# Kernel tuning notes

Measured on AMD Instinct MI355X. Metric: run time of the kernel, lower is better.

The kernel has to match this reference:

```python
import jax, jax.numpy as jnp
import numpy as np

N_PTS = 2_097_152


def _pe(x):
    # num_frequencies = 3: [sin(pi x), cos(pi x), sin(2pi x), cos(2pi x), sin(4pi x), cos(4pi x)] -> [N,18]
    parts = []
    for i in range(3):
        f = np.float32((2.0 ** i) * np.pi)
        parts.append(jnp.sin(f * x))
        parts.append(jnp.cos(f * x))
    return jnp.concatenate(parts, axis=-1)


def _trilinear(vol, coords):
    # vol: [C,D,H,W]; coords: [N,3] in grid_sample order (x->W, y->H, z->D),
    # align_corners=False, zeros padding. Returns [C,N].
    C, D, H, W = vol.shape
    x = (coords[:, 0] + 1.0) * (W * 0.5) - 0.5
    y = (coords[:, 1] + 1.0) * (H * 0.5) - 0.5
    z = (coords[:, 2] + 1.0) * (D * 0.5) - 0.5
    x0f = jnp.floor(x); y0f = jnp.floor(y); z0f = jnp.floor(z)
    tx = x - x0f; ty = y - y0f; tz = z - z0f
    x0 = x0f.astype(jnp.int32); y0 = y0f.astype(jnp.int32); z0 = z0f.astype(jnp.int32)

    def corner(zi, yi, xi, w):
        valid = (zi >= 0) & (zi < D) & (yi >= 0) & (yi < H) & (xi >= 0) & (xi < W)
        v = vol[:, jnp.clip(zi, 0, D - 1), jnp.clip(yi, 0, H - 1), jnp.clip(xi, 0, W - 1)]
        return v * (w * valid)[None, :]

    return (corner(z0, y0, x0, (1 - tz) * (1 - ty) * (1 - tx))
            + corner(z0, y0, x0 + 1, (1 - tz) * (1 - ty) * tx)
            + corner(z0, y0 + 1, x0, (1 - tz) * ty * (1 - tx))
            + corner(z0, y0 + 1, x0 + 1, (1 - tz) * ty * tx)
            + corner(z0 + 1, y0, x0, tz * (1 - ty) * (1 - tx))
            + corner(z0 + 1, y0, x0 + 1, tz * (1 - ty) * tx)
            + corner(z0 + 1, y0 + 1, x0, tz * ty * (1 - tx))
            + corner(z0 + 1, y0 + 1, x0 + 1, tz * ty * tx))


def setup_inputs() -> dict:
    key = jax.random.key(0)
    ks = jax.random.split(key, 11)
    q = 1.0
    inp = {
        'x': jax.random.uniform(ks[0], (N_PTS, 3), dtype=jnp.float32),
        'grid0': jax.random.normal(ks[1], (4, 32, 32, 32), dtype=jnp.float32),
        'grid1': jax.random.normal(ks[2], (4, 64, 64, 64), dtype=jnp.float32),
        'grid2': jax.random.normal(ks[3], (2, 128, 128, 128), dtype=jnp.float32),
        'noise0': jax.random.uniform(ks[4], (4, 32, 32, 32), dtype=jnp.float32) / q - 0.5 / q,
        'noise1': jax.random.uniform(ks[5], (4, 64, 64, 64), dtype=jnp.float32) / q - 0.5 / q,
        'noise2': jax.random.uniform(ks[6], (2, 128, 128, 128), dtype=jnp.float32) / q - 0.5 / q,
        'w1': jax.random.normal(ks[7], (64, 20), dtype=jnp.float32) * (1.0 / np.sqrt(20.0)),
        'b1': jnp.zeros((64,), dtype=jnp.float32),
        'w2': jax.random.normal(ks[8], (7, 64), dtype=jnp.float32) * (1.0 / np.sqrt(64.0)),
        'b2': jnp.zeros((7,), dtype=jnp.float32),
    }
    return inp


def reference(x, grid0, grid1, grid2, noise0, noise1, noise2, w1, b1, w2, b2):
    pe = _pe(x)  # [N,18]
    feats = []
    for i, (g, nz) in enumerate(((grid0, noise0), (grid1, noise1), (grid2, noise2))):
        gv = g + nz  # training-mode noise injection, shared across the two samples
        feats.append(_trilinear(gv, pe[:, i * 6:i * 6 + 3]))
        feats.append(_trilinear(gv, pe[:, i * 6 + 3:i * 6 + 6]))
    f = jnp.concatenate(feats, axis=0).T  # [N,20]
    h = jax.nn.leaky_relu(f @ w1.T + b1, negative_slope=0.01)
    return h @ w2.T + b2  # [N,7]
```

## Files before the change

kernel.cpp:

```cpp
#include <hip/hip_runtime.h>


#define NB 16384
#define KB 128
#define NXCD 8

typedef _Float16 f16x2 __attribute__((ext_vector_type(2)));
typedef __fp16  h8    __attribute__((ext_vector_type(8)));
typedef float   f4    __attribute__((ext_vector_type(4)));

__device__ __forceinline__ f16x2 pkrtz(float a, float b) {
    return __builtin_bit_cast(f16x2, __builtin_amdgcn_cvt_pkrtz(a, b));
}
__device__ __forceinline__ unsigned pkrtzu(float a, float b) {
    return __builtin_bit_cast(unsigned, __builtin_amdgcn_cvt_pkrtz(a, b));
}
__device__ __forceinline__ float fdot2(f16x2 a, f16x2 b, float c) {
    return __builtin_amdgcn_fdot2(a, b, c, false);
}
__device__ __forceinline__ f16x2 u2h(unsigned u) { return __builtin_bit_cast(f16x2, u); }

__device__ __forceinline__ int bin_of(float xv, float yv, float zv) {
    int qx = min(max((int)(xv * 16.f), 0), 15);
    int qy = min(max((int)(yv * 32.f), 0), 31);
    int qz = min(max((int)(zv * 32.f), 0), 31);
    return (qz << 9) | (qy << 4) | qx;
}

#define PREP_BLOCKS 9568

__global__ __launch_bounds__(256)
void prep_k(const float* __restrict__ x,
            const float* __restrict__ g0, const float* __restrict__ n0,
            const float* __restrict__ g1, const float* __restrict__ n1,
            const float* __restrict__ g2, const float* __restrict__ n2,
            const float* __restrict__ w1, const float* __restrict__ w2,
            uint2* __restrict__ p0, uint2* __restrict__ p1,
            unsigned* __restrict__ p2,
            unsigned short* __restrict__ w1p, unsigned short* __restrict__ w2p,
            int* __restrict__ counts, int npts) {
    __shared__ unsigned h32[NB / 2];
    const int b = blockIdx.x, t = threadIdx.x;
    if (b < 8256) {
        int i = b * 256 + t;
        if (i < 2113536) {
            int z = i / 16512, rem = i % 16512;
            int y = rem / 129, xp = rem % 129;
            int v = (z * 128 + y) * 128 + max(xp - 1, 0);
            p2[i] = pkrtzu(g2[v] + n2[v], g2[2097152 + v] + n2[2097152 + v]);
        }
    } else if (b < 9296) {
        int i = (b - 8256) * 256 + t;
        if (i < 266240) {
            int z = i / 4160, rem = i % 4160;
            int y = rem / 65, xp = rem % 65;
            int v = (z * 64 + y) * 64 + max(xp - 1, 0);
            uint2 r;
            r.x = pkrtzu(g1[v] + n1[v], g1[262144 + v] + n1[262144 + v]);
            r.y = pkrtzu(g1[524288 + v] + n1[524288 + v], g1[786432 + v] + n1[786432 + v]);
            p1[i] = r;
        }
    } else if (b < 9428) {
        int i = (b - 9296) * 256 + t;
        if (i < 33792) {
            int z = i / 1056, rem = i % 1056;
            int y = rem / 33, xp = rem % 33;
            int v = (z * 32 + y) * 32 + max(xp - 1, 0);
            uint2 r;
            r.x = pkrtzu(g0[v] + n0[v], g0[32768 + v] + n0[32768 + v]);
            r.y = pkrtzu(g0[65536 + v] + n0[65536 + v], g0[98304 + v] + n0[98304 + v]);
            p0[i] = r;
        }
    } else if (b < 9556) {
        const int cb = b - 9428;
        for (int i = t; i < NB / 2; i += 256) h32[i] = 0u;
        __syncthreads();
        const int chunk = (npts + KB - 1) / KB;
        const int s = cb * chunk, e = min(s + chunk, npts);
        for (int p = s + t; p < e; p += 256) {
            int bin = bin_of(x[3 * p], x[3 * p + 1], x[3 * p + 2]);
            atomicAdd(&h32[bin >> 1], 1u << ((bin & 1) * 16));
        }
        __syncthreads();
        for (int i = t; i < NB; i += 256)
            counts[cb * NB + i] = (int)((h32[i >> 1] >> ((i & 1) * 16)) & 0xffffu);
    } else {
        int i = (b - 9556) * 256 + t;
        if (i < 2048) {
            int j = i >> 5, k = i & 31;
            float v = (k < 20) ? w1[j * 20 + k] : 0.f;
            w1p[i] = __builtin_bit_cast(unsigned short, (_Float16)v);
        } else if (i < 3072) {
            int i2 = i - 2048;
            int o = i2 >> 6, jj = i2 & 63;
            float v = (o < 7) ? w2[o * 64 + jj] : 0.f;
            w2p[i2] = __builtin_bit_cast(unsigned short, (_Float16)v);
        }
    }
}

__global__ __launch_bounds__(256)
void scan_rows_k(const int* __restrict__ counts, int* __restrict__ offs,
                 int* __restrict__ rowsum) {
    __shared__ int tile[KB][32];
    const int g = blockIdx.x, t = threadIdx.x;
    for (int idx = t; idx < KB * 32; idx += 256) {
        int b = idx >> 5, j = idx & 31;
        tile[b][j] = counts[b * NB + g * 32 + j];
    }
    __syncthreads();
    if (t < 32) {
        int run = 0;
#pragma unroll 8
        for (int b = 0; b < KB; ++b) {
            int v = tile[b][t];
            tile[b][t] = run;
            run += v;
        }
        rowsum[g * 32 + t] = run;
    }
    __syncthreads();
    for (int idx = t; idx < KB * 32; idx += 256) {
        int b = idx >> 5, j = idx & 31;
        offs[b * NB + g * 32 + j] = tile[b][j];
    }
}

__global__ __launch_bounds__(1024)
void scatter_k(const float* __restrict__ x, const int* __restrict__ offs,
               const int* __restrict__ rowsum, float4* __restrict__ sorted,
               int npts) {
    __shared__ int base[NB];
    __shared__ int sh[1024];
    const int t = threadIdx.x, b = blockIdx.x;

    int s16 = 0;
    for (int i = 0; i < 16; ++i) s16 += rowsum[t * 16 + i];
    sh[t] = s16;
    __syncthreads();
    for (int d = 1; d < 1024; d <<= 1) {
        int add = (t >= d) ? sh[t - d] : 0;
        __syncthreads();
        sh[t] += add;
        __syncthreads();
    }
    int run = sh[t] - s16;
    for (int i = 0; i < 16; ++i) {
        int v = rowsum[t * 16 + i];
        base[t * 16 + i] = run;
        run += v;
    }
    __syncthreads();
    for (int i = t; i < NB; i += 1024) base[i] += offs[b * NB + i];
    __syncthreads();

    const int chunk = (npts + KB - 1) / KB;
    const int s = b * chunk, e = min(s + chunk, npts);
    for (int p = s + t; p < e; p += 1024) {
        float xv = x[3 * p], yv = x[3 * p + 1], zv = x[3 * p + 2];
        int pos = atomicAdd(&base[bin_of(xv, yv, zv)], 1);
        float4 v; v.x = xv; v.y = yv; v.z = zv; v.w = __int_as_float(p);
        sorted[pos] = v;
    }
}

template<int S>
__device__ __forceinline__ void tl_setup(float cx, float cy, float cz,
        int& o00, int& o01, int& o10, int& o11,
        f16x2& w00, f16x2& w01, f16x2& w10, f16x2& w11) {
    const float hs = (float)S * 0.5f;
    float gx = fmaf(cx, hs, hs - 0.5f);
    float gy = fmaf(cy, hs, hs - 0.5f);
    float gz = fmaf(cz, hs, hs - 0.5f);
    float fx = floorf(gx), fy = floorf(gy), fz = floorf(gz);
    float tx = gx - fx, ty = gy - fy, tz = gz - fz;
    int x0 = (int)fx, y0 = (int)fy, z0 = (int)fz;
    float wx0 = (1.f - tx) * ((x0 >= 0)    ? 1.f : 0.f);
    float wx1 = tx         * ((x0 + 1 < S) ? 1.f : 0.f);
    float wy0 = (1.f - ty) * ((y0 >= 0)    ? 1.f : 0.f);
    float wy1 = ty         * ((y0 + 1 < S) ? 1.f : 0.f);
    float wz0 = (1.f - tz) * ((z0 >= 0)    ? 1.f : 0.f);
    float wz1 = tz         * ((z0 + 1 < S) ? 1.f : 0.f);
    const int xb = x0 + 1;
    f16x2 wx2 = pkrtz(wx0, wx1);
    int ys0 = max(y0, 0), ys1 = min(y0 + 1, S - 1);
    int zs0 = max(z0, 0), zs1 = min(z0 + 1, S - 1);
    o00 = (zs0 * S + ys0) * (S + 1) + xb;
    o01 = (zs0 * S + ys1) * (S + 1) + xb;
    o10 = (zs1 * S + ys0) * (S + 1) + xb;
    o11 = (zs1 * S + ys1) * (S + 1) + xb;
    float a00 = wz0 * wy0, a01 = wz0 * wy1, a10 = wz1 * wy0, a11 = wz1 * wy1;
    w00 = pkrtz(a00, a00) * wx2;
    w01 = pkrtz(a01, a01) * wx2;
    w10 = pkrtz(a10, a10) * wx2;
    w11 = pkrtz(a11, a11) * wx2;
}

struct TL4S {
    uint4 r00, r01, r10, r11;
    f16x2 w00, w01, w10, w11;
};
template<int S>
__device__ __forceinline__ TL4S tl4_issue(const uint2* __restrict__ vol,
                                          float cx, float cy, float cz) {
    TL4S r; int o00, o01, o10, o11;
    tl_setup<S>(cx, cy, cz, o00, o01, o10, o11, r.w00, r.w01, r.w10, r.w11);
    r.r00 = *reinterpret_cast<const uint4*>(vol + o00);
    r.r01 = *reinterpret_cast<const uint4*>(vol + o01);
    r.r10 = *reinterpret_cast<const uint4*>(vol + o10);
    r.r11 = *reinterpret_cast<const uint4*>(vol + o11);
    return r;
}
#define TL4_ROW(s, R, WP, f) { uint4 r = (s).R; \
    unsigned pc0 = __builtin_amdgcn_perm(r.z, r.x, 0x05040100u); \
    unsigned pc1 = __builtin_amdgcn_perm(r.z, r.x, 0x07060302u); \
    unsigned pc2 = __builtin_amdgcn_perm(r.w, r.y, 0x05040100u); \
    unsigned pc3 = __builtin_amdgcn_perm(r.w, r.y, 0x07060302u); \
    (f)[0] = fdot2((s).WP, u2h(pc0), (f)[0]); (f)[1] = fdot2((s).WP, u2h(pc1), (f)[1]); \
    (f)[2] = fdot2((s).WP, u2h(pc2), (f)[2]); (f)[3] = fdot2((s).WP, u2h(pc3), (f)[3]); }
__device__ __forceinline__ void tl4_consume(const TL4S& s, float* f) {
    TL4_ROW(s, r00, w00, f) TL4_ROW(s, r01, w01, f)
    TL4_ROW(s, r10, w10, f) TL4_ROW(s, r11, w11, f)
}

struct TL2S {
    uint2 r00, r01, r10, r11;
    f16x2 w00, w01, w10, w11;
};
template<int S>
__device__ __forceinline__ TL2S tl2_issue(const unsigned* __restrict__ vol,
                                          float cx, float cy, float cz) {
    TL2S r; int o00, o01, o10, o11;
    tl_setup<S>(cx, cy, cz, o00, o01, o10, o11, r.w00, r.w01, r.w10, r.w11);
    r.r00 = *reinterpret_cast<const uint2*>(vol + o00);
    r.r01 = *reinterpret_cast<const uint2*>(vol + o01);
    r.r10 = *reinterpret_cast<const uint2*>(vol + o10);
    r.r11 = *reinterpret_cast<const uint2*>(vol + o11);
    return r;
}
#define TL2_ROW(s, R, WP, f) { uint2 r = (s).R; \
    unsigned pc0 = __builtin_amdgcn_perm(r.y, r.x, 0x05040100u); \
    unsigned pc1 = __builtin_amdgcn_perm(r.y, r.x, 0x07060302u); \
    (f)[0] = fdot2((s).WP, u2h(pc0), (f)[0]); (f)[1] = fdot2((s).WP, u2h(pc1), (f)[1]); }
__device__ __forceinline__ void tl2_consume(const TL2S& s, float* f) {
    TL2_ROW(s, r00, w00, f) TL2_ROW(s, r01, w01, f)
    TL2_ROW(s, r10, w10, f) TL2_ROW(s, r11, w11, f)
}

__device__ __forceinline__ void trig3(float x, float y, float z,
        float* s1, float* c1, float* s2, float* c2, float* s4, float* c4) {
    const float v[3] = {x, y, z};
#pragma unroll
    for (int d = 0; d < 3; ++d) {
        float sa = __builtin_amdgcn_sinf(0.5f * v[d]);
        float ca = __builtin_amdgcn_cosf(0.5f * v[d]);
        s1[d] = sa; c1[d] = ca;
        float sb = 2.f * sa * ca, cb = fmaf(-2.f * sa, sa, 1.f);
        s2[d] = sb; c2[d] = cb;
        s4[d] = 2.f * sb * cb; c4[d] = fmaf(-2.f * sb, sb, 1.f);
    }
}

__global__ __launch_bounds__(256, 3)
void motion_grid_main(const float4* __restrict__ sorted,
                      const float* __restrict__ xraw,
                      const uint2* __restrict__ g0v,
                      const uint2* __restrict__ g1v,
                      const unsigned* __restrict__ g2v,
                      const unsigned short* __restrict__ w1p_,
                      const unsigned short* __restrict__ w2p_,
                      const float* __restrict__ b1,
                      const float* __restrict__ b2,
                      float* __restrict__ out, int npts, int sortedMode,
                      int nblk) {
    __shared__ __align__(16) char smem[4 * 7424];
    int bid = blockIdx.x;
    if ((nblk & (NXCD - 1)) == 0) {
        int cpx = nblk / NXCD;
        bid = (bid % NXCD) * cpx + bid / NXCD;
    }
    const int tid = threadIdx.x;
    const int w = tid >> 6, l = tid & 63, c = l & 15, g = l >> 4;
    char* wbase = smem + w * 7424;
    const int p = bid * 256 + tid;

    float xv = 0.f, yv = 0.f, zv = 0.f;
    int orig = -1;
    if (p < npts) {
        if (sortedMode) {
            float4 sp = sorted[p];
            xv = sp.x; yv = sp.y; zv = sp.z; orig = __float_as_int(sp.w);
        } else {
            xv = xraw[3 * p]; yv = xraw[3 * p + 1]; zv = xraw[3 * p + 2];
            orig = p;
        }
    }
    float s1[3], c1[3], s2[3], c2[3], s4[3], c4[3];
    trig3(xv, yv, zv, s1, c1, s2, c2, s4, c4);

    TL4S S0s = tl4_issue<32>(g0v, s1[0], s1[1], s1[2]);
    TL4S S0c = tl4_issue<32>(g0v, c1[0], c1[1], c1[2]);
    TL4S S1s = tl4_issue<64>(g1v, s2[0], s2[1], s2[2]);
    TL4S S1c = tl4_issue<64>(g1v, c2[0], c2[1], c2[2]);
    TL2S S2s = tl2_issue<128>(g2v, s4[0], s4[1], s4[2]);
    TL2S S2c = tl2_issue<128>(g2v, c4[0], c4[1], c4[2]);

    float f[20];
#pragma unroll
    for (int i = 0; i < 20; ++i) f[i] = 0.f;
    tl4_consume(S0s, f + 0);  tl4_consume(S0c, f + 4);
    tl4_consume(S1s, f + 8);  tl4_consume(S1c, f + 12);
    tl2_consume(S2s, f + 16); tl2_consume(S2c, f + 18);
    {
        uint4* fs = (uint4*)(wbase + l * 80);
        fs[0] = make_uint4(pkrtzu(f[0], f[1]), pkrtzu(f[2], f[3]),
                           pkrtzu(f[4], f[5]), pkrtzu(f[6], f[7]));
        fs[1] = make_uint4(pkrtzu(f[8], f[9]), pkrtzu(f[10], f[11]),
                           pkrtzu(f[12], f[13]), pkrtzu(f[14], f[15]));
        fs[2] = make_uint4(pkrtzu(f[16], f[17]), pkrtzu(f[18], f[19]), 0u, 0u);
        fs[3] = make_uint4(0u, 0u, 0u, 0u);
    }

    h8 a1f0 = *(const h8*)(w1p_ + (0 * 16 + c) * 32 + g * 8);
    h8 a1f1 = *(const h8*)(w1p_ + (1 * 16 + c) * 32 + g * 8);
    h8 a1f2 = *(const h8*)(w1p_ + (2 * 16 + c) * 32 + g * 8);
    h8 a1f3 = *(const h8*)(w1p_ + (3 * 16 + c) * 32 + g * 8);
    f4 b1f0 = *(const f4*)(b1 + 0 * 16 + g * 4);
    f4 b1f1 = *(const f4*)(b1 + 1 * 16 + g * 4);
    f4 b1f2 = *(const f4*)(b1 + 2 * 16 + g * 4);
    f4 b1f3 = *(const f4*)(b1 + 3 * 16 + g * 4);
    h8 a20 = *(const h8*)(w2p_ + c * 64 + g * 8);
    h8 a21 = *(const h8*)(w2p_ + c * 64 + 32 + g * 8);
    float b2f0 = (g * 4 + 0 < 7) ? b2[g * 4 + 0] : 0.f;
    float b2f1 = (g * 4 + 1 < 7) ? b2[g * 4 + 1] : 0.f;
    float b2f2 = (g * 4 + 2 < 7) ? b2[g * 4 + 2] : 0.f;
    float b2f3 = (g * 4 + 3 < 7) ? b2[g * 4 + 3] : 0.f;

    const f4 zero4 = {0.f, 0.f, 0.f, 0.f};
#pragma unroll
    for (int n = 0; n < 4; ++n) {
        h8 bn = *(const h8*)(wbase + (n * 16 + c) * 80 + g * 16);
        __builtin_amdgcn_s_setprio(1);
        f4 d0 = __builtin_amdgcn_mfma_f32_16x16x32_f16(a1f0, bn, zero4, 0, 0, 0);
        f4 d1 = __builtin_amdgcn_mfma_f32_16x16x32_f16(a1f1, bn, zero4, 0, 0, 0);
        f4 d2m = __builtin_amdgcn_mfma_f32_16x16x32_f16(a1f2, bn, zero4, 0, 0, 0);
        f4 d3 = __builtin_amdgcn_mfma_f32_16x16x32_f16(a1f3, bn, zero4, 0, 0, 0);
        __builtin_amdgcn_s_setprio(0);
        d0 += b1f0; d1 += b1f1; d2m += b1f2; d3 += b1f3;
        {
            float h0 = fmaxf(d0[0], 0.01f * d0[0]), h1 = fmaxf(d0[1], 0.01f * d0[1]);
            float h2 = fmaxf(d0[2], 0.01f * d0[2]), h3 = fmaxf(d0[3], 0.01f * d0[3]);
            *(uint2*)(wbase + 5120 + c * 144 + 0 * 32 + g * 8) =
                make_uint2(pkrtzu(h0, h1), pkrtzu(h2, h3));
            h0 = fmaxf(d1[0], 0.01f * d1[0]); h1 = fmaxf(d1[1], 0.01f * d1[1]);
            h2 = fmaxf(d1[2], 0.01f * d1[2]); h3 = fmaxf(d1[3], 0.01f * d1[3]);
            *(uint2*)(wbase + 5120 + c * 144 + 1 * 32 + g * 8) =
                make_uint2(pkrtzu(h0, h1), pkrtzu(h2, h3));
            h0 = fmaxf(d2m[0], 0.01f * d2m[0]); h1 = fmaxf(d2m[1], 0.01f * d2m[1]);
            h2 = fmaxf(d2m[2], 0.01f * d2m[2]); h3 = fmaxf(d2m[3], 0.01f * d2m[3]);
            *(uint2*)(wbase + 5120 + c * 144 + 2 * 32 + g * 8) =
                make_uint2(pkrtzu(h0, h1), pkrtzu(h2, h3));
            h0 = fmaxf(d3[0], 0.01f * d3[0]); h1 = fmaxf(d3[1], 0.01f * d3[1]);
            h2 = fmaxf(d3[2], 0.01f * d3[2]); h3 = fmaxf(d3[3], 0.01f * d3[3]);
            *(uint2*)(wbase + 5120 + c * 144 + 3 * 32 + g * 8) =
                make_uint2(pkrtzu(h0, h1), pkrtzu(h2, h3));
        }
        h8 hb0 = *(const h8*)(wbase + 5120 + c * 144 + g * 16);
        h8 hb1 = *(const h8*)(wbase + 5120 + c * 144 + 64 + g * 16);
        __builtin_amdgcn_s_setprio(1);
        f4 o2 = __builtin_amdgcn_mfma_f32_16x16x32_f16(a20, hb0, zero4, 0, 0, 0);
        o2 = __builtin_amdgcn_mfma_f32_16x16x32_f16(a21, hb1, o2, 0, 0, 0);
        __builtin_amdgcn_s_setprio(0);
        int og = __shfl(orig, n * 16 + c, 64);
        if (og >= 0 && g < 2) {
            float* op = out + (size_t)og * 7 + g * 4;
            op[0] = o2[0] + b2f0;
            op[1] = o2[1] + b2f1;
            op[2] = o2[2] + b2f2;
            if (g == 0) op[3] = o2[3] + b2f3;
        }
    }
}

extern "C" void kernel_launch(void* const* d_in, const int* in_sizes, int n_in,
                              void* d_out, int out_size, void* d_ws, size_t ws_size,
                              hipStream_t stream) {
    const float* x  = (const float*)d_in[0];
    const float* g0 = (const float*)d_in[1];
    const float* g1 = (const float*)d_in[2];
    const float* g2 = (const float*)d_in[3];
    const float* n0 = (const float*)d_in[4];
    const float* n1 = (const float*)d_in[5];
    const float* n2 = (const float*)d_in[6];
    const float* w1 = (const float*)d_in[7];
    const float* b1 = (const float*)d_in[8];
    const float* w2 = (const float*)d_in[9];
    const float* b2 = (const float*)d_in[10];
    float* out = (float*)d_out;

    const int npts = in_sizes[0] / 3;

    char* ws = (char*)d_ws;
    size_t cur = 0;
    auto alloc = [&](size_t bytes) {
        char* p = ws + cur;
        cur = (cur + bytes + 255) & ~(size_t)255;
        return p;
    };
    uint2*          p0       = (uint2*)         alloc(33792u   * 8 + 64);
    uint2*          p1       = (uint2*)         alloc(266240u  * 8 + 64);
    unsigned*       p2       = (unsigned*)      alloc(2113536u * 4 + 64);
    unsigned short* w1p      = (unsigned short*)alloc(2048 * 2);
    unsigned short* w2p      = (unsigned short*)alloc(1024 * 2);
    int*            counts   = (int*)           alloc((size_t)KB * NB * 4);
    int*            offs     = (int*)           alloc((size_t)KB * NB * 4);
    int*            rowsum   = (int*)           alloc(NB * 4);
    float4*         sorted   = (float4*)        alloc((size_t)npts * 16);
    const int useSorted = (ws_size >= cur) ? 1 : 0;

    prep_k<<<PREP_BLOCKS, 256, 0, stream>>>(x, g0, n0, g1, n1, g2, n2, w1, w2,
                                            p0, p1, p2, w1p, w2p, counts, npts);
    if (useSorted) {
        scan_rows_k<<<NB / 32, 256, 0, stream>>>(counts, offs, rowsum);
        scatter_k<<<KB, 1024, 0, stream>>>(x, offs, rowsum, sorted, npts);
    }

    const int nblk = (npts + 255) / 256;
    motion_grid_main<<<nblk, 256, 0, stream>>>(
        sorted, x, p0, p1, p2, w1p, w2p, b1, b2, out, npts, useSorted, nblk);
}
```

Baseline: 198.8 us.

## Refine spatial binning to 32K bins and split histogram into its own kernel

Changes the point-sorting grid from 16x32x32 to 8x64x64 bins (32768 total) for finer y/z locality in the later trilinear gathers. Moves the histogram out of prep_k into a separate 1024-thread kernel, reuses the counts buffer in place for offsets instead of a separate offs array, and replaces the block-wide scan in scatter_k with a wavefront shuffle scan. This adds a kernel launch and doubles the per-block count traffic and the LDS use of scatter_k, in exchange for potentially better cache locality in the main kernel.

Result: faster. 172.1 us, median of 2 (-13.4%).

```diff
diff --git a/kernel.cpp b/kernel.cpp
--- a/kernel.cpp
+++ b/kernel.cpp
@@ -1,7 +1,7 @@
 #include <hip/hip_runtime.h>
 
 
-#define NB 16384
+#define NB 32768
 #define KB 128
 #define NXCD 8
 
@@ -21,25 +21,22 @@
 __device__ __forceinline__ f16x2 u2h(unsigned u) { return __builtin_bit_cast(f16x2, u); }
 
 __device__ __forceinline__ int bin_of(float xv, float yv, float zv) {
-    int qx = min(max((int)(xv * 16.f), 0), 15);
-    int qy = min(max((int)(yv * 32.f), 0), 31);
-    int qz = min(max((int)(zv * 32.f), 0), 31);
-    return (qz << 9) | (qy << 4) | qx;
-}
-
-#define PREP_BLOCKS 9568
+    int qx = min(max((int)(xv * 8.f), 0), 7);
+    int qy = min(max((int)(yv * 64.f), 0), 63);
+    int qz = min(max((int)(zv * 64.f), 0), 63);
+    return (qz << 9) | (qy << 3) | qx;
+}
+
+#define PREP_BLOCKS 9440
 
 __global__ __launch_bounds__(256)
-void prep_k(const float* __restrict__ x,
-            const float* __restrict__ g0, const float* __restrict__ n0,
+void prep_k(const float* __restrict__ g0, const float* __restrict__ n0,
             const float* __restrict__ g1, const float* __restrict__ n1,
             const float* __restrict__ g2, const float* __restrict__ n2,
             const float* __restrict__ w1, const float* __restrict__ w2,
             uint2* __restrict__ p0, uint2* __restrict__ p1,
             unsigned* __restrict__ p2,
-            unsigned short* __restrict__ w1p, unsigned short* __restrict__ w2p,
-            int* __restrict__ counts, int npts) {
-    __shared__ unsigned h32[NB / 2];
+            unsigned short* __restrict__ w1p, unsigned short* __restrict__ w2p) {
     const int b = blockIdx.x, t = threadIdx.x;
     if (b < 8256) {
         int i = b * 256 + t;
@@ -71,21 +68,8 @@
             r.y = pkrtzu(g0[65536 + v] + n0[65536 + v], g0[98304 + v] + n0[98304 + v]);
             p0[i] = r;
         }
-    } else if (b < 9556) {
-        const int cb = b - 9428;
-        for (int i = t; i < NB / 2; i += 256) h32[i] = 0u;
-        __syncthreads();
-        const int chunk = (npts + KB - 1) / KB;
-        const int s = cb * chunk, e = min(s + chunk, npts);
-        for (int p = s + t; p < e; p += 256) {
-            int bin = bin_of(x[3 * p], x[3 * p + 1], x[3 * p + 2]);
-            atomicAdd(&h32[bin >> 1], 1u << ((bin & 1) * 16));
-        }
-        __syncthreads();
-        for (int i = t; i < NB; i += 256)
-            counts[cb * NB + i] = (int)((h32[i >> 1] >> ((i & 1) * 16)) & 0xffffu);
     } else {
-        int i = (b - 9556) * 256 + t;
+        int i = (b - 9428) * 256 + t;
         if (i < 2048) {
             int j = i >> 5, k = i & 31;
             float v = (k < 20) ? w1[j * 20 + k] : 0.f;
@@ -99,9 +83,25 @@
     }
 }
 
+__global__ __launch_bounds__(1024)
+void hist_k(const float* __restrict__ x, int* __restrict__ counts, int npts) {
+    __shared__ unsigned h32[NB / 2];
+    const int t = threadIdx.x, b = blockIdx.x;
+    for (int i = t; i < NB / 2; i += 1024) h32[i] = 0u;
+    __syncthreads();
+    const int chunk = (npts + KB - 1) / KB;
+    const int s = b * chunk, e = min(s + chunk, npts);
+    for (int p = s + t; p < e; p += 1024) {
+        int bin = bin_of(x[3 * p], x[3 * p + 1], x[3 * p + 2]);
+        atomicAdd(&h32[bin >> 1], 1u << ((bin & 1) * 16));
+    }
+    __syncthreads();
+    for (int i = t; i < NB; i += 1024)
+        counts[b * NB + i] = (int)((h32[i >> 1] >> ((i & 1) * 16)) & 0xffffu);
+}
+
 __global__ __launch_bounds__(256)
-void scan_rows_k(const int* __restrict__ counts, int* __restrict__ offs,
-                 int* __restrict__ rowsum) {
+void scan_rows_k(int* __restrict__ counts, int* __restrict__ rowsum) {
     __shared__ int tile[KB][32];
     const int g = blockIdx.x, t = threadIdx.x;
     for (int idx = t; idx < KB * 32; idx += 256) {
@@ -122,7 +122,7 @@
     __syncthreads();
     for (int idx = t; idx < KB * 32; idx += 256) {
         int b = idx >> 5, j = idx & 31;
-        offs[b * NB + g * 32 + j] = tile[b][j];
+        counts[b * NB + g * 32 + j] = tile[b][j];
     }
 }
 
@@ -131,23 +131,29 @@
                const int* __restrict__ rowsum, float4* __restrict__ sorted,
                int npts) {
     __shared__ int base[NB];
-    __shared__ int sh[1024];
+    __shared__ int wsum[16];
     const int t = threadIdx.x, b = blockIdx.x;
-
-    int s16 = 0;
-    for (int i = 0; i < 16; ++i) s16 += rowsum[t * 16 + i];
-    sh[t] = s16;
-    __syncthreads();
-    for (int d = 1; d < 1024; d <<= 1) {
-        int add = (t >= d) ? sh[t - d] : 0;
-        __syncthreads();
-        sh[t] += add;
-        __syncthreads();
-    }
-    int run = sh[t] - s16;
-    for (int i = 0; i < 16; ++i) {
-        int v = rowsum[t * 16 + i];
-        base[t * 16 + i] = run;
+    const int lane = t & 63;
+
+    const int t32 = t * 32;
+    int s32 = 0;
+    for (int i = 0; i < 32; ++i) s32 += rowsum[t32 + i];
+    int inc = s32;
+    for (int d = 1; d < 64; d <<= 1) {
+        int o = __shfl_up(inc, d, 64);
+        if (lane >= d) inc += o;
+    }
+    if (lane == 63) wsum[t >> 6] = inc;
+    __syncthreads();
+    if (t == 0) {
+        int acc = 0;
+        for (int i = 0; i < 16; ++i) { int v = wsum[i]; wsum[i] = acc; acc += v; }
+    }
+    __syncthreads();
+    int run = wsum[t >> 6] + inc - s32;
+    for (int i = 0; i < 32; ++i) {
+        int v = rowsum[t32 + i];
+        base[t32 + i] = run;
         run += v;
     }
     __syncthreads();
@@ -413,16 +419,16 @@
     unsigned short* w1p      = (unsigned short*)alloc(2048 * 2);
     unsigned short* w2p      = (unsigned short*)alloc(1024 * 2);
     int*            counts   = (int*)           alloc((size_t)KB * NB * 4);
-    int*            offs     = (int*)           alloc((size_t)KB * NB * 4);
     int*            rowsum   = (int*)           alloc(NB * 4);
     float4*         sorted   = (float4*)        alloc((size_t)npts * 16);
     const int useSorted = (ws_size >= cur) ? 1 : 0;
 
-    prep_k<<<PREP_BLOCKS, 256, 0, stream>>>(x, g0, n0, g1, n1, g2, n2, w1, w2,
-                                            p0, p1, p2, w1p, w2p, counts, npts);
+    prep_k<<<PREP_BLOCKS, 256, 0, stream>>>(g0, n0, g1, n1, g2, n2, w1, w2,
+                                            p0, p1, p2, w1p, w2p);
     if (useSorted) {
-        scan_rows_k<<<NB / 32, 256, 0, stream>>>(counts, offs, rowsum);
-        scatter_k<<<KB, 1024, 0, stream>>>(x, offs, rowsum, sorted, npts);
+        hist_k<<<KB, 1024, 0, stream>>>(x, counts, npts);
+        scan_rows_k<<<NB / 32, 256, 0, stream>>>(counts, rowsum);
+        scatter_k<<<KB, 1024, 0, stream>>>(x, counts, rowsum, sorted, npts);
     }
 
     const int nblk = (npts + 255) / 256;
```
